# Kernel optimization log

Hardware: AMD Instinct MI355X
Metric: run time of the kernel (lower is better)

## Reference

```python
import jax, jax.numpy as jnp
import numpy as np

B, T, I, H = 64, 1024, 256, 256

def setup_inputs() -> dict:
    key = jax.random.key(0)
    ks = jax.random.split(key, 7)
    inputs = jax.random.normal(ks[0], (B * T, I), jnp.float32)
    states = jax.random.normal(ks[1], (B, 1, H), jnp.float32)  # [B, num_layers, H]
    mask = (jax.random.uniform(ks[2], (B, T, 1, 1)) < 0.9).astype(jnp.float32)
    s = 1.0 / np.sqrt(H)  # PyTorch RNN init scale
    W_ih = jax.random.uniform(ks[3], (3 * H, I), jnp.float32, -s, s)
    W_hh = jax.random.uniform(ks[4], (3 * H, H), jnp.float32, -s, s)
    b_ih = jax.random.uniform(ks[5], (3 * H,), jnp.float32, -s, s)
    b_hh = jax.random.uniform(ks[6], (3 * H,), jnp.float32, -s, s)
    return dict(inputs=inputs, states=states, mask=mask,
                W_ih=W_ih, W_hh=W_hh, b_ih=b_ih, b_hh=b_hh, seq_len=T)

def reference(inputs, states, mask, W_ih, W_hh, b_ih, b_hh, seq_len):
    # inputs: [B*T, I] -> [B, T, I]
    x = inputs.reshape(-1, seq_len, inputs.shape[-1])
    m = mask[..., 0, 0]                      # [B, T]
    # pre-loop blend: hs = states * mask[:, 0]
    h0 = states[:, 0, :] * m[:, 0:1]         # [B, H]
    xs = jnp.swapaxes(x, 0, 1)               # [T, B, I]
    ms = jnp.swapaxes(m, 0, 1)[..., None]    # [T, B, 1]

    def step(h, xm):
        x_t, m_t = xm
        gi = x_t @ W_ih.T + b_ih             # [B, 3H]
        gh = h @ W_hh.T + b_hh               # [B, 3H]
        ir, iz, i_n = jnp.split(gi, 3, axis=-1)
        hr, hz, h_n = jnp.split(gh, 3, axis=-1)
        r = jax.nn.sigmoid(ir + hr)
        z = jax.nn.sigmoid(iz + hz)
        n = jnp.tanh(i_n + r * h_n)
        nh = (1.0 - z) * n + z * h           # GRU new hidden = step output
        h_new = h * (1.0 - m_t) + nh * m_t   # masked state blend
        return h_new, nh

    h_fin, ys = jax.lax.scan(step, h0, (xs, ms))
    x_out = jnp.swapaxes(ys, 0, 1).reshape(-1, ys.shape[-1])  # [B*T, H]
    state_out = h_fin[:, None, :]                              # [B, 1, H]
    return (x_out, state_out)
```

## Files before the change

### kernel.cpp

```cpp
#include <hip/hip_runtime.h>

typedef unsigned int u32;
typedef __fp16 f16;
typedef __fp16 h2 __attribute__((ext_vector_type(2)));
typedef __fp16 h8 __attribute__((ext_vector_type(8)));
typedef float f32x2v __attribute__((ext_vector_type(2)));
typedef float f32x4v __attribute__((ext_vector_type(4)));
typedef float f32x16v __attribute__((ext_vector_type(16)));
typedef u32 u32x4v __attribute__((ext_vector_type(4)));

static constexpr int BB = 64;
static constexpr int TT = 1024;
static constexpr int HH = 256;
static constexpr int GG = 768;
static constexpr size_t GI_BYTES = (size_t)BB * TT * GG * 2;

__device__ __forceinline__ u32 pk2(float a, float b) {
  h2 r = __builtin_amdgcn_cvt_pkrtz(a, b);
  return __builtin_bit_cast(u32, r);
}
__device__ __forceinline__ float fdot2u(u32 a, u32 b, float c) {
  return __builtin_amdgcn_fdot2(__builtin_bit_cast(h2, a), __builtin_bit_cast(h2, b), c, false);
}
__device__ __forceinline__ float dpp_x1(float x) {
  return __builtin_bit_cast(float,
      __builtin_amdgcn_mov_dpp(__builtin_bit_cast(int, x), 0xB1, 0xF, 0xF, true));
}
__device__ __forceinline__ float sigf(float x) { return 1.f / (1.f + __expf(-x)); }
__device__ __forceinline__ float tanhf2(float x) {
  float e = __expf(2.f * x);
  return 1.f - 2.f / (e + 1.f);
}

__global__ void prepack_whh(const float* __restrict__ Whh, u32* __restrict__ Wp) {
  int id = blockIdx.x * 256 + threadIdx.x;
  int v = id >> 9;
  int j = id & 511;
  int u = j >> 1, kh = j & 1;
  int g = v >> 6, d = v & 63;
  int row = g * 256 + u;
  int k0 = 128 * kh + 2 * d;
  const float* p = Whh + (size_t)row * HH + k0;
  Wp[id] = pk2(p[0], p[1]);
}

__device__ __forceinline__ f32x16v zero16() {
  f32x16v z;
#pragma unroll
  for (int i = 0; i < 16; ++i) z[i] = 0.f;
  return z;
}

__global__ __launch_bounds__(256, 2) void gemm_gi(
    const float* __restrict__ x, const float* __restrict__ Wih,
    const float* __restrict__ bih, f16* __restrict__ gi) {
  __shared__ u32 bl[16384];
  const int tid = threadIdx.x;
  const int lane = tid & 63;
  const int wv = tid >> 6;
  const int wr = wv >> 1, wc = wv & 1;
  const int l31 = lane & 31, lh = lane >> 5;
  const int m0 = blockIdx.x << 7;

  u32x4v afr[2][16];
#pragma unroll
  for (int fr = 0; fr < 2; ++fr) {
#pragma unroll
    for (int km = 0; km < 16; ++km) {
      int row = m0 + wr * 64 + fr * 32 + l31;
      int k0 = km * 16 + lh * 8;
      const f32x4v* p = (const f32x4v*)(x + (size_t)row * 256 + k0);
      f32x4v u = p[0], v = p[1];
      u32x4v t;
      t.x = pk2(u.x, u.y); t.y = pk2(u.z, u.w);
      t.z = pk2(v.x, v.y); t.w = pk2(v.z, v.w);
      afr[fr][km] = t;
    }
  }

  for (int nt = 0; nt < 6; ++nt) {
    const int n0 = nt << 7;
#pragma unroll
    for (int i = 0; i < 64; ++i) {
      int idx = i * 256 + tid;
      int r = idx >> 7, wd = idx & 127;
      const f32x2v* g = (const f32x2v*)(Wih + (size_t)(n0 + r) * 256 + 2 * wd);
      f32x2v f = *g;
      bl[r * 128 + (wd ^ ((r & 15) << 2))] = pk2(f.x, f.y);
    }
    __syncthreads();

    f32x16v acc00 = zero16(), acc01 = zero16(), acc10 = zero16(), acc11 = zero16();
#pragma unroll
    for (int km = 0; km < 16; ++km) {
      int w0 = km * 8 + lh * 4;
      int rc0 = wc * 64 + l31;
      int rc1 = wc * 64 + 32 + l31;
      u32x4v b0 = *(const u32x4v*)&bl[rc0 * 128 + (w0 ^ ((rc0 & 15) << 2))];
      u32x4v b1 = *(const u32x4v*)&bl[rc1 * 128 + (w0 ^ ((rc1 & 15) << 2))];
      h8 a0h = __builtin_bit_cast(h8, afr[0][km]);
      h8 a1h = __builtin_bit_cast(h8, afr[1][km]);
      h8 b0h = __builtin_bit_cast(h8, b0);
      h8 b1h = __builtin_bit_cast(h8, b1);
      acc00 = __builtin_amdgcn_mfma_f32_32x32x16_f16(a0h, b0h, acc00, 0, 0, 0);
      acc10 = __builtin_amdgcn_mfma_f32_32x32x16_f16(a1h, b0h, acc10, 0, 0, 0);
      acc01 = __builtin_amdgcn_mfma_f32_32x32x16_f16(a0h, b1h, acc01, 0, 0, 0);
      acc11 = __builtin_amdgcn_mfma_f32_32x32x16_f16(a1h, b1h, acc11, 0, 0, 0);
    }

#define EPI(ACC, FR, FC)                                                      \
    {                                                                         \
      int gc = n0 + wc * 64 + (FC) * 32 + l31;                                \
      float bias = bih[gc];                                                   \
      _Pragma("unroll")                                                       \
      for (int rg = 0; rg < 16; ++rg) {                                       \
        int gr = m0 + wr * 64 + (FR) * 32 + 4 * lh + (rg & 3) + 8 * (rg >> 2);\
        gi[(size_t)gr * 768 + gc] = (f16)(ACC[rg] + bias);                    \
      }                                                                       \
    }
    EPI(acc00, 0, 0) EPI(acc10, 1, 0) EPI(acc01, 0, 1) EPI(acc11, 1, 1)
#undef EPI
    __syncthreads();
  }
}

__global__ __launch_bounds__(512, 2) void recur(
    const u32* __restrict__ Wp, const f16* __restrict__ gi,
    const float* __restrict__ states, const float* __restrict__ mask,
    const float* __restrict__ bhh_g, float* __restrict__ out) {
  const int b = blockIdx.x;
  const int j = threadIdx.x;
  const int u = j >> 1;
  const int kh = j & 1;

  __shared__ u32 hbuf[2][128];
  __shared__ float mlds[TT];

  u32 w[192];
#pragma unroll
  for (int v = 0; v < 192; ++v) w[v] = Wp[(size_t)v * 512 + j];
#pragma unroll
  for (int v = 0; v < 192; ++v) asm volatile("" : "+v"(w[v]));

  const float bhr = bhh_g[u];
  const float bhz = bhh_g[256 + u];
  const float bhn = bhh_g[512 + u];

  const float* mk = mask + b * TT;
  const f16* gib = gi + (size_t)b * TT * GG;
  float* outb = out + (size_t)b * TT * HH;

  for (int i = j; i < TT; i += 512) mlds[i] = mk[i];

  float hreg = states[b * HH + u] * mk[0];
  if (kh == 0) ((f16*)hbuf[0])[u] = (f16)hreg;
  __syncthreads();

  f16 gr_c = gib[u], gz_c = gib[256 + u], gn_c = gib[512 + u];
  float nh_prev = 0.f;

  for (int t = 0; t < TT; ++t) {
    int tn = (t + 1 < TT) ? (t + 1) : (TT - 1);
    const f16* gnp = gib + (size_t)tn * GG;
    f16 gr_n = gnp[u], gz_n = gnp[256 + u], gn_n = gnp[512 + u];
    if (t > 0 && kh == 0) outb[(size_t)(t - 1) * HH + u] = nh_prev;

    const float mt = mlds[t];
    const u32x4v* hq = (const u32x4v*)&hbuf[t & 1][kh << 6];

    float ar0 = 0.f, ar1 = 0.f, az0 = 0.f, az1 = 0.f, an0 = 0.f, an1 = 0.f;
#pragma unroll
    for (int gp = 0; gp < 16; ++gp) {
      u32x4v q = hq[gp];
      const int v = gp * 4;
      ar0 = fdot2u(w[v + 0], q.x, ar0);
      az0 = fdot2u(w[64 + v + 0], q.x, az0);
      an0 = fdot2u(w[128 + v + 0], q.x, an0);
      ar1 = fdot2u(w[v + 1], q.y, ar1);
      az1 = fdot2u(w[64 + v + 1], q.y, az1);
      an1 = fdot2u(w[128 + v + 1], q.y, an1);
      ar0 = fdot2u(w[v + 2], q.z, ar0);
      az0 = fdot2u(w[64 + v + 2], q.z, az0);
      an0 = fdot2u(w[128 + v + 2], q.z, an0);
      ar1 = fdot2u(w[v + 3], q.w, ar1);
      az1 = fdot2u(w[64 + v + 3], q.w, az1);
      an1 = fdot2u(w[128 + v + 3], q.w, an1);
    }
    float ghr = ar0 + ar1, ghz = az0 + az1, ghn = an0 + an1;
    ghr += dpp_x1(ghr); ghz += dpp_x1(ghz); ghn += dpp_x1(ghn);
    ghr += bhr; ghz += bhz; ghn += bhn;

    float r = sigf((float)gr_c + ghr);
    float z = sigf((float)gz_c + ghz);
    float n = tanhf2((float)gn_c + r * ghn);
    float nh = (1.f - z) * n + z * hreg;
    float hnew = hreg * (1.f - mt) + nh * mt;
    nh_prev = nh;
    hreg = hnew;
    if (kh == 0) ((f16*)hbuf[(t + 1) & 1])[u] = (f16)hnew;
    gr_c = gr_n; gz_c = gz_n; gn_c = gn_n;
    __syncthreads();
  }

  if (kh == 0) {
    outb[(size_t)(TT - 1) * HH + u] = nh_prev;
    out[(size_t)BB * TT * HH + b * HH + u] = hreg;
  }
}

extern "C" void kernel_launch(void* const* d_in, const int* in_sizes, int n_in,
                              void* d_out, int out_size, void* d_ws, size_t ws_size,
                              hipStream_t stream) {
  const float* x      = (const float*)d_in[0];
  const float* states = (const float*)d_in[1];
  const float* mask   = (const float*)d_in[2];
  const float* W_ih   = (const float*)d_in[3];
  const float* W_hh   = (const float*)d_in[4];
  const float* b_ih   = (const float*)d_in[5];
  const float* b_hh   = (const float*)d_in[6];
  float* out = (float*)d_out;

  char* ws = (char*)d_ws;
  f16* gi = (f16*)ws;
  u32* Wp = (u32*)(ws + GI_BYTES);

  prepack_whh<<<dim3(384), dim3(256), 0, stream>>>(W_hh, Wp);
  gemm_gi<<<dim3(512), dim3(256), 0, stream>>>(x, W_ih, b_ih, gi);
  recur<<<dim3(64), dim3(512), 0, stream>>>(Wp, gi, states, mask, b_hh, out);
}
```

Baseline: 1.541 ms.

## Batch eight sequences per block and compute recurrent GEMV with MFMA

The recurrent kernel now handles 8 batch rows per block (8 blocks instead of 64). The h·W_hh product becomes 16x16x32 f16 MFMA instructions with W_hh prepacked into AGPR-resident fragments, replacing per-thread fdot2 chains. The r/z recurrent biases are folded into the input GEMM epilogue, and the W_ih staging load is widened to float4. The intent is to cut per-step dot-product cost by using matrix units. The trade-off is only 8 active CUs and more per-step work per block, all still serialized on the recurrence.

```diff
diff --git a/kernel.cpp b/kernel.cpp
--- a/kernel.cpp
+++ b/kernel.cpp
@@ -3,10 +3,12 @@
 typedef unsigned int u32;
 typedef __fp16 f16;
 typedef __fp16 h2 __attribute__((ext_vector_type(2)));
+typedef __fp16 h4 __attribute__((ext_vector_type(4)));
 typedef __fp16 h8 __attribute__((ext_vector_type(8)));
 typedef float f32x2v __attribute__((ext_vector_type(2)));
 typedef float f32x4v __attribute__((ext_vector_type(4)));
 typedef float f32x16v __attribute__((ext_vector_type(16)));
+typedef u32 u32x2v __attribute__((ext_vector_type(2)));
 typedef u32 u32x4v __attribute__((ext_vector_type(4)));
 
 static constexpr int BB = 64;
@@ -19,12 +21,9 @@
   h2 r = __builtin_amdgcn_cvt_pkrtz(a, b);
   return __builtin_bit_cast(u32, r);
 }
-__device__ __forceinline__ float fdot2u(u32 a, u32 b, float c) {
-  return __builtin_amdgcn_fdot2(__builtin_bit_cast(h2, a), __builtin_bit_cast(h2, b), c, false);
-}
-__device__ __forceinline__ float dpp_x1(float x) {
+__device__ __forceinline__ float dpp_shr8(float x) {
   return __builtin_bit_cast(float,
-      __builtin_amdgcn_mov_dpp(__builtin_bit_cast(int, x), 0xB1, 0xF, 0xF, true));
+      __builtin_amdgcn_mov_dpp(__builtin_bit_cast(int, x), 0x118, 0xF, 0xF, true));
 }
 __device__ __forceinline__ float sigf(float x) { return 1.f / (1.f + __expf(-x)); }
 __device__ __forceinline__ float tanhf2(float x) {
@@ -32,16 +31,19 @@
   return 1.f - 2.f / (e + 1.f);
 }
 
-__global__ void prepack_whh(const float* __restrict__ Whh, u32* __restrict__ Wp) {
+__global__ void prepack_wa(const float* __restrict__ Whh, u32* __restrict__ Wa) {
   int id = blockIdx.x * 256 + threadIdx.x;
-  int v = id >> 9;
-  int j = id & 511;
-  int u = j >> 1, kh = j & 1;
-  int g = v >> 6, d = v & 63;
-  int row = g * 256 + u;
-  int k0 = 128 * kh + 2 * d;
-  const float* p = Whh + (size_t)row * HH + k0;
-  Wp[id] = pk2(p[0], p[1]);
+  int lane_g = id / 192;
+  int rrem = id - lane_g * 192;
+  int i = rrem >> 2, e2 = rrem & 3;
+  int ti6 = i >> 3, ks = i & 7;
+  int G = ti6 >> 1, tj = ti6 & 1;
+  int w = lane_g >> 6, l = lane_g & 63;
+  int m = G * 16 + 2 * w + tj;
+  int row = 16 * m + (l & 15);
+  int k = 32 * ks + 8 * (l >> 4) + 2 * e2;
+  const float* p = Whh + (size_t)row * HH + k;
+  Wa[id] = pk2(p[0], p[1]);
 }
 
 __device__ __forceinline__ f32x16v zero16() {
@@ -53,7 +55,8 @@
 
 __global__ __launch_bounds__(256, 2) void gemm_gi(
     const float* __restrict__ x, const float* __restrict__ Wih,
-    const float* __restrict__ bih, f16* __restrict__ gi) {
+    const float* __restrict__ bih, const float* __restrict__ bhh,
+    f16* __restrict__ gi) {
   __shared__ u32 bl[16384];
   const int tid = threadIdx.x;
   const int lane = tid & 63;
@@ -81,12 +84,16 @@
   for (int nt = 0; nt < 6; ++nt) {
     const int n0 = nt << 7;
 #pragma unroll
-    for (int i = 0; i < 64; ++i) {
-      int idx = i * 256 + tid;
-      int r = idx >> 7, wd = idx & 127;
-      const f32x2v* g = (const f32x2v*)(Wih + (size_t)(n0 + r) * 256 + 2 * wd);
-      f32x2v f = *g;
-      bl[r * 128 + (wd ^ ((r & 15) << 2))] = pk2(f.x, f.y);
+    for (int it = 0; it < 32; ++it) {
+      int flat = it * 256 + tid;
+      int r = flat >> 6;
+      int q = flat & 63;
+      f32x4v f = *(const f32x4v*)(Wih + (size_t)(n0 + r) * 256 + 4 * q);
+      u32x2v pw;
+      pw.x = pk2(f.x, f.y);
+      pw.y = pk2(f.z, f.w);
+      int wd = 2 * q;
+      *(u32x2v*)&bl[r * 128 + (wd ^ ((r & 15) << 2))] = pw;
     }
     __syncthreads();
 
@@ -111,7 +118,7 @@
 #define EPI(ACC, FR, FC)                                                      \
     {                                                                         \
       int gc = n0 + wc * 64 + (FC) * 32 + l31;                                \
-      float bias = bih[gc];                                                   \
+      float bias = bih[gc] + (gc < 512 ? bhh[gc] : 0.f);                      \
       _Pragma("unroll")                                                       \
       for (int rg = 0; rg < 16; ++rg) {                                       \
         int gr = m0 + wr * 64 + (FR) * 32 + 4 * lh + (rg & 3) + 8 * (rg >> 2);\
@@ -125,87 +132,117 @@
 }
 
 __global__ __launch_bounds__(512, 2) void recur(
-    const u32* __restrict__ Wp, const f16* __restrict__ gi,
+    const u32* __restrict__ Wa, const f16* __restrict__ gi,
     const float* __restrict__ states, const float* __restrict__ mask,
     const float* __restrict__ bhh_g, float* __restrict__ out) {
-  const int b = blockIdx.x;
-  const int j = threadIdx.x;
-  const int u = j >> 1;
-  const int kh = j & 1;
-
-  __shared__ u32 hbuf[2][128];
-  __shared__ float mlds[TT];
-
-  u32 w[192];
-#pragma unroll
-  for (int v = 0; v < 192; ++v) w[v] = Wp[(size_t)v * 512 + j];
-#pragma unroll
-  for (int v = 0; v < 192; ++v) asm volatile("" : "+v"(w[v]));
-
-  const float bhr = bhh_g[u];
-  const float bhz = bhh_g[256 + u];
-  const float bhn = bhh_g[512 + u];
-
-  const float* mk = mask + b * TT;
-  const f16* gib = gi + (size_t)b * TT * GG;
-  float* outb = out + (size_t)b * TT * HH;
-
-  for (int i = j; i < TT; i += 512) mlds[i] = mk[i];
-
-  float hreg = states[b * HH + u] * mk[0];
-  if (kh == 0) ((f16*)hbuf[0])[u] = (f16)hreg;
+  const int blk = blockIdx.x;
+  const int tid = threadIdx.x;
+  const int w = tid >> 6, l = tid & 63;
+  const int lr = l & 15, g = l >> 4;
+  const int c = lr & 7, tj = lr >> 3;
+  const int u0 = 32 * w + 16 * tj + 4 * g;
+
+  __shared__ __align__(16) f16 hb[2][4096];
+  __shared__ f16 mlds[8192];
+
+  u32x4v wa[48];
+  {
+    const u32x4v* wap = (const u32x4v*)Wa + (size_t)(w * 64 + l) * 48;
+#pragma unroll
+    for (int i = 0; i < 48; ++i) wa[i] = wap[i];
+#pragma unroll
+    for (int i = 0; i < 48; ++i) asm volatile("" : "+a"(wa[i]));
+  }
+
+  for (int idx = tid; idx < 8192; idx += 512) {
+    int b8 = idx >> 10, tt = idx & 1023;
+    mlds[tt * 8 + b8] = (f16)mask[(size_t)(blk * 8 + b8) * TT + tt];
+  }
+  for (int idx = tid; idx < 4096; idx += 512) {
+    int unit = idx >> 4, cc = idx & 15;
+    float v = 0.f;
+    if (cc < 8)
+      v = states[(size_t)(blk * 8 + cc) * HH + unit] *
+          mask[(size_t)(blk * 8 + cc) * TT];
+    int fa = (unit >> 5) * 512 + ((unit >> 3) & 3) * 128 + cc * 8 + (unit & 7);
+    hb[0][fa] = (f16)v;
+    hb[1][fa] = (f16)v;
+  }
+
+  const f16* gip = gi + (size_t)(blk * 8 + c) * TT * GG + u0;
+  float* outp = out + (size_t)(blk * 8 + c) * TT * HH + u0;
+
+  float hreg[4];
+  {
+    float m0 = mask[(size_t)(blk * 8 + c) * TT];
+    const f32x4v s4 = *(const f32x4v*)(states + (size_t)(blk * 8 + c) * HH + u0);
+#pragma unroll
+    for (int r = 0; r < 4; ++r) hreg[r] = s4[r] * m0;
+  }
+  const f32x4v bn4 = *(const f32x4v*)(bhh_g + 512 + u0);
+
+  const int wbase = w * 512 + ((2 * tj + (g >> 1)) & 3) * 128 + c * 8 + 4 * (g & 1);
+  const int rbase = g * 128 + lr * 8;
+
+  f32x4v nhp = {0.f, 0.f, 0.f, 0.f};
   __syncthreads();
 
-  f16 gr_c = gib[u], gz_c = gib[256 + u], gn_c = gib[512 + u];
-  float nh_prev = 0.f;
-
   for (int t = 0; t < TT; ++t) {
-    int tn = (t + 1 < TT) ? (t + 1) : (TT - 1);
-    const f16* gnp = gib + (size_t)tn * GG;
-    f16 gr_n = gnp[u], gz_n = gnp[256 + u], gn_n = gnp[512 + u];
-    if (t > 0 && kh == 0) outb[(size_t)(t - 1) * HH + u] = nh_prev;
-
-    const float mt = mlds[t];
-    const u32x4v* hq = (const u32x4v*)&hbuf[t & 1][kh << 6];
-
-    float ar0 = 0.f, ar1 = 0.f, az0 = 0.f, az1 = 0.f, an0 = 0.f, an1 = 0.f;
-#pragma unroll
-    for (int gp = 0; gp < 16; ++gp) {
-      u32x4v q = hq[gp];
-      const int v = gp * 4;
-      ar0 = fdot2u(w[v + 0], q.x, ar0);
-      az0 = fdot2u(w[64 + v + 0], q.x, az0);
-      an0 = fdot2u(w[128 + v + 0], q.x, an0);
-      ar1 = fdot2u(w[v + 1], q.y, ar1);
-      az1 = fdot2u(w[64 + v + 1], q.y, az1);
-      an1 = fdot2u(w[128 + v + 1], q.y, an1);
-      ar0 = fdot2u(w[v + 2], q.z, ar0);
-      az0 = fdot2u(w[64 + v + 2], q.z, az0);
-      an0 = fdot2u(w[128 + v + 2], q.z, an0);
-      ar1 = fdot2u(w[v + 3], q.w, ar1);
-      az1 = fdot2u(w[64 + v + 3], q.w, az1);
-      an1 = fdot2u(w[128 + v + 3], q.w, an1);
-    }
-    float ghr = ar0 + ar1, ghz = az0 + az1, ghn = an0 + an1;
-    ghr += dpp_x1(ghr); ghz += dpp_x1(ghz); ghn += dpp_x1(ghn);
-    ghr += bhr; ghz += bhz; ghn += bhn;
-
-    float r = sigf((float)gr_c + ghr);
-    float z = sigf((float)gz_c + ghz);
-    float n = tanhf2((float)gn_c + r * ghn);
-    float nh = (1.f - z) * n + z * hreg;
-    float hnew = hreg * (1.f - mt) + nh * mt;
-    nh_prev = nh;
-    hreg = hnew;
-    if (kh == 0) ((f16*)hbuf[(t + 1) & 1])[u] = (f16)hnew;
-    gr_c = gr_n; gz_c = gz_n; gn_c = gn_n;
+    if (t > 0) *(f32x4v*)(outp + (size_t)(t - 1) * HH) = nhp;
+    const h4 ldA = *(const h4*)(gip + (size_t)t * GG);
+    const h4 ldB = *(const h4*)(gip + (size_t)t * GG + 256);
+    const h4 ldC = *(const h4*)(gip + (size_t)t * GG + 512);
+    const float mt = (float)mlds[t * 8 + c];
+
+    const u32x4v* bp = (const u32x4v*)&hb[t & 1][rbase];
+    f32x4v a0 = {0.f, 0.f, 0.f, 0.f}, a1 = a0, a2 = a0, a3 = a0, a4 = a0, a5 = a0;
+    u32x4v bf = bp[0];
+#pragma unroll
+    for (int ks = 0; ks < 8; ++ks) {
+      u32x4v bnx = bp[((ks + 1) & 7) * 64];
+      h8 bh = __builtin_bit_cast(h8, bf);
+      a0 = __builtin_amdgcn_mfma_f32_16x16x32_f16(__builtin_bit_cast(h8, wa[ks]),      bh, a0, 0, 0, 0);
+      a1 = __builtin_amdgcn_mfma_f32_16x16x32_f16(__builtin_bit_cast(h8, wa[8 + ks]),  bh, a1, 0, 0, 0);
+      a2 = __builtin_amdgcn_mfma_f32_16x16x32_f16(__builtin_bit_cast(h8, wa[16 + ks]), bh, a2, 0, 0, 0);
+      a3 = __builtin_amdgcn_mfma_f32_16x16x32_f16(__builtin_bit_cast(h8, wa[24 + ks]), bh, a3, 0, 0, 0);
+      a4 = __builtin_amdgcn_mfma_f32_16x16x32_f16(__builtin_bit_cast(h8, wa[32 + ks]), bh, a4, 0, 0, 0);
+      a5 = __builtin_amdgcn_mfma_f32_16x16x32_f16(__builtin_bit_cast(h8, wa[40 + ks]), bh, a5, 0, 0, 0);
+      bf = bnx;
+    }
+
+    const bool hi = (lr >= 8);
+    f32x4v vr, vz, vn;
+#pragma unroll
+    for (int r = 0; r < 4; ++r) {
+      float d0 = dpp_shr8(a1[r]);
+      float d1 = dpp_shr8(a3[r]);
+      float d2 = dpp_shr8(a5[r]);
+      vr[r] = hi ? d0 : a0[r];
+      vz[r] = hi ? d1 : a2[r];
+      vn[r] = hi ? d2 : a4[r];
+    }
+
+#pragma unroll
+    for (int r = 0; r < 4; ++r) {
+      float rr = sigf((float)ldA[r] + vr[r]);
+      float zz = sigf((float)ldB[r] + vz[r]);
+      float nn = tanhf2((float)ldC[r] + rr * (vn[r] + bn4[r]));
+      float nh = zz * (hreg[r] - nn) + nn;
+      hreg[r] = hreg[r] + mt * (nh - hreg[r]);
+      nhp[r] = nh;
+    }
+    u32x2v hp;
+    hp.x = pk2(hreg[0], hreg[1]);
+    hp.y = pk2(hreg[2], hreg[3]);
+    *(u32x2v*)&hb[(t + 1) & 1][wbase] = hp;
     __syncthreads();
   }
 
-  if (kh == 0) {
-    outb[(size_t)(TT - 1) * HH + u] = nh_prev;
-    out[(size_t)BB * TT * HH + b * HH + u] = hreg;
-  }
+  *(f32x4v*)(outp + (size_t)(TT - 1) * HH) = nhp;
+  f32x4v hf;
+#pragma unroll
+  for (int r = 0; r < 4; ++r) hf[r] = hreg[r];
+  *(f32x4v*)(out + (size_t)BB * TT * HH + (size_t)(blk * 8 + c) * HH + u0) = hf;
 }
 
 extern "C" void kernel_launch(void* const* d_in, const int* in_sizes, int n_in,
@@ -222,9 +259,9 @@
 
   char* ws = (char*)d_ws;
   f16* gi = (f16*)ws;
-  u32* Wp = (u32*)(ws + GI_BYTES);
-
-  prepack_whh<<<dim3(384), dim3(256), 0, stream>>>(W_hh, Wp);
-  gemm_gi<<<dim3(512), dim3(256), 0, stream>>>(x, W_ih, b_ih, gi);
-  recur<<<dim3(64), dim3(512), 0, stream>>>(Wp, gi, states, mask, b_hh, out);
-}
+  u32* Wa = (u32*)(ws + GI_BYTES);
+
+  prepack_wa<<<dim3(384), dim3(256), 0, stream>>>(W_hh, Wa);
+  gemm_gi<<<dim3(512), dim3(256), 0, stream>>>(x, W_ih, b_ih, b_hh, gi);
+  recur<<<dim3(8), dim3(512), 0, stream>>>(Wa, gi, states, mask, b_hh, out);
+}
```

After: 2.739 ms. 1.78x slower.

## Pin recurrent weights to fixed VGPRs via inline asm and fold biases into GEMM

Applied to the files above, without the earlier changes.

The recurrent kernel now loads its 192 packed W_hh words per thread straight into hard-wired VGPRs v64-v255 with inline-asm dwordx4 loads. The dot products are written as inline v_dot2 asm, so the compiler can no longer spill or shuffle the weights, and the per-thread weight layout is repacked to be contiguous for wide loads. The r/z hidden biases are folded into the input GEMM epilogue, the GRU blend math is simplified, and the W_ih staging loads are widened to float4. The software prefetch of next-step gi values is removed, so each step now loads gi on the critical path. Relying on fixed register numbers with clobbers is fragile and may conflict with compiler allocation.

```diff
diff --git a/kernel.cpp b/kernel.cpp
--- a/kernel.cpp
+++ b/kernel.cpp
@@ -1,12 +1,14 @@
 #include <hip/hip_runtime.h>
 
 typedef unsigned int u32;
+typedef unsigned long long u64;
 typedef __fp16 f16;
 typedef __fp16 h2 __attribute__((ext_vector_type(2)));
 typedef __fp16 h8 __attribute__((ext_vector_type(8)));
 typedef float f32x2v __attribute__((ext_vector_type(2)));
 typedef float f32x4v __attribute__((ext_vector_type(4)));
 typedef float f32x16v __attribute__((ext_vector_type(16)));
+typedef u32 u32x2v __attribute__((ext_vector_type(2)));
 typedef u32 u32x4v __attribute__((ext_vector_type(4)));
 
 static constexpr int BB = 64;
@@ -19,9 +21,6 @@
   h2 r = __builtin_amdgcn_cvt_pkrtz(a, b);
   return __builtin_bit_cast(u32, r);
 }
-__device__ __forceinline__ float fdot2u(u32 a, u32 b, float c) {
-  return __builtin_amdgcn_fdot2(__builtin_bit_cast(h2, a), __builtin_bit_cast(h2, b), c, false);
-}
 __device__ __forceinline__ float dpp_x1(float x) {
   return __builtin_bit_cast(float,
       __builtin_amdgcn_mov_dpp(__builtin_bit_cast(int, x), 0xB1, 0xF, 0xF, true));
@@ -32,16 +31,14 @@
   return 1.f - 2.f / (e + 1.f);
 }
 
-__global__ void prepack_whh(const float* __restrict__ Whh, u32* __restrict__ Wp) {
+__global__ void prepack_whh(const float* __restrict__ Whh, u32* __restrict__ Wp2) {
   int id = blockIdx.x * 256 + threadIdx.x;
-  int v = id >> 9;
-  int j = id & 511;
+  int j = id / 192;
+  int rem = id - j * 192;
+  int G = rem >> 6, d = rem & 63;
   int u = j >> 1, kh = j & 1;
-  int g = v >> 6, d = v & 63;
-  int row = g * 256 + u;
-  int k0 = 128 * kh + 2 * d;
-  const float* p = Whh + (size_t)row * HH + k0;
-  Wp[id] = pk2(p[0], p[1]);
+  const float* p = Whh + (size_t)(G * 256 + u) * HH + 128 * kh + 2 * d;
+  Wp2[id] = pk2(p[0], p[1]);
 }
 
 __device__ __forceinline__ f32x16v zero16() {
@@ -53,7 +50,8 @@
 
 __global__ __launch_bounds__(256, 2) void gemm_gi(
     const float* __restrict__ x, const float* __restrict__ Wih,
-    const float* __restrict__ bih, f16* __restrict__ gi) {
+    const float* __restrict__ bih, const float* __restrict__ bhh,
+    f16* __restrict__ gi) {
   __shared__ u32 bl[16384];
   const int tid = threadIdx.x;
   const int lane = tid & 63;
@@ -81,12 +79,16 @@
   for (int nt = 0; nt < 6; ++nt) {
     const int n0 = nt << 7;
 #pragma unroll
-    for (int i = 0; i < 64; ++i) {
-      int idx = i * 256 + tid;
-      int r = idx >> 7, wd = idx & 127;
-      const f32x2v* g = (const f32x2v*)(Wih + (size_t)(n0 + r) * 256 + 2 * wd);
-      f32x2v f = *g;
-      bl[r * 128 + (wd ^ ((r & 15) << 2))] = pk2(f.x, f.y);
+    for (int it = 0; it < 32; ++it) {
+      int flat = it * 256 + tid;
+      int r = flat >> 6;
+      int q = flat & 63;
+      f32x4v f = *(const f32x4v*)(Wih + (size_t)(n0 + r) * 256 + 4 * q);
+      u32x2v pw;
+      pw.x = pk2(f.x, f.y);
+      pw.y = pk2(f.z, f.w);
+      int wd = 2 * q;
+      *(u32x2v*)&bl[r * 128 + (wd ^ ((r & 15) << 2))] = pw;
     }
     __syncthreads();
 
@@ -111,7 +113,7 @@
 #define EPI(ACC, FR, FC)                                                      \
     {                                                                         \
       int gc = n0 + wc * 64 + (FC) * 32 + l31;                                \
-      float bias = bih[gc];                                                   \
+      float bias = bih[gc] + (gc < 512 ? bhh[gc] : 0.f);                      \
       _Pragma("unroll")                                                       \
       for (int rg = 0; rg < 16; ++rg) {                                       \
         int gr = m0 + wr * 64 + (FR) * 32 + 4 * lh + (rg & 3) + 8 * (rg >> 2);\
@@ -124,8 +126,54 @@
   }
 }
 
+#define WCLOB \
+  "v64","v65","v66","v67","v68","v69","v70","v71", \
+  "v72","v73","v74","v75","v76","v77","v78","v79", \
+  "v80","v81","v82","v83","v84","v85","v86","v87", \
+  "v88","v89","v90","v91","v92","v93","v94","v95", \
+  "v96","v97","v98","v99","v100","v101","v102","v103", \
+  "v104","v105","v106","v107","v108","v109","v110","v111", \
+  "v112","v113","v114","v115","v116","v117","v118","v119", \
+  "v120","v121","v122","v123","v124","v125","v126","v127", \
+  "v128","v129","v130","v131","v132","v133","v134","v135", \
+  "v136","v137","v138","v139","v140","v141","v142","v143", \
+  "v144","v145","v146","v147","v148","v149","v150","v151", \
+  "v152","v153","v154","v155","v156","v157","v158","v159", \
+  "v160","v161","v162","v163","v164","v165","v166","v167", \
+  "v168","v169","v170","v171","v172","v173","v174","v175", \
+  "v176","v177","v178","v179","v180","v181","v182","v183", \
+  "v184","v185","v186","v187","v188","v189","v190","v191", \
+  "v192","v193","v194","v195","v196","v197","v198","v199", \
+  "v200","v201","v202","v203","v204","v205","v206","v207", \
+  "v208","v209","v210","v211","v212","v213","v214","v215", \
+  "v216","v217","v218","v219","v220","v221","v222","v223", \
+  "v224","v225","v226","v227","v228","v229","v230","v231", \
+  "v232","v233","v234","v235","v236","v237","v238","v239", \
+  "v240","v241","v242","v243","v244","v245","v246","v247", \
+  "v248","v249","v250","v251","v252","v253","v254","v255"
+
+#define LD16(A,B,OFF) "global_load_dwordx4 v[" #A ":" #B "], %0, off offset:" #OFF "\n\t"
+
+#define DOTG(R0,R1,R2,R3,Z0,Z1,Z2,Z3,N0,N1,N2,N3,Q)          \
+  asm volatile(                                              \
+    "v_dot2_f32_f16 %0, v" #R0 ", %3, %0\n\t"                \
+    "v_dot2_f32_f16 %1, v" #Z0 ", %3, %1\n\t"                \
+    "v_dot2_f32_f16 %2, v" #N0 ", %3, %2\n\t"                \
+    "v_dot2_f32_f16 %0, v" #R1 ", %4, %0\n\t"                \
+    "v_dot2_f32_f16 %1, v" #Z1 ", %4, %1\n\t"                \
+    "v_dot2_f32_f16 %2, v" #N1 ", %4, %2\n\t"                \
+    "v_dot2_f32_f16 %0, v" #R2 ", %5, %0\n\t"                \
+    "v_dot2_f32_f16 %1, v" #Z2 ", %5, %1\n\t"                \
+    "v_dot2_f32_f16 %2, v" #N2 ", %5, %2\n\t"                \
+    "v_dot2_f32_f16 %0, v" #R3 ", %6, %0\n\t"                \
+    "v_dot2_f32_f16 %1, v" #Z3 ", %6, %1\n\t"                \
+    "v_dot2_f32_f16 %2, v" #N3 ", %6, %2\n\t"                \
+    : "+v"(ar), "+v"(az), "+v"(an)                           \
+    : "v"((Q).x), "v"((Q).y), "v"((Q).z), "v"((Q).w)         \
+    : WCLOB)
+
 __global__ __launch_bounds__(512, 2) void recur(
-    const u32* __restrict__ Wp, const f16* __restrict__ gi,
+    const u32* __restrict__ Wp2, const f16* __restrict__ gi,
     const float* __restrict__ states, const float* __restrict__ mask,
     const float* __restrict__ bhh_g, float* __restrict__ out) {
   const int b = blockIdx.x;
@@ -133,72 +181,80 @@
   const int u = j >> 1;
   const int kh = j & 1;
 
-  __shared__ u32 hbuf[2][128];
+  __shared__ __align__(16) u32 hbuf[2][128];
   __shared__ float mlds[TT];
 
-  u32 w[192];
-#pragma unroll
-  for (int v = 0; v < 192; ++v) w[v] = Wp[(size_t)v * 512 + j];
-#pragma unroll
-  for (int v = 0; v < 192; ++v) asm volatile("" : "+v"(w[v]));
-
-  const float bhr = bhh_g[u];
-  const float bhz = bhh_g[256 + u];
   const float bhn = bhh_g[512 + u];
 
   const float* mk = mask + b * TT;
-  const f16* gib = gi + (size_t)b * TT * GG;
+  const f16* gcur = gi + (size_t)b * TT * GG + u;
   float* outb = out + (size_t)b * TT * HH;
 
   for (int i = j; i < TT; i += 512) mlds[i] = mk[i];
 
   float hreg = states[b * HH + u] * mk[0];
   if (kh == 0) ((f16*)hbuf[0])[u] = (f16)hreg;
+
+  {
+    u64 wa = (u64)(Wp2 + (size_t)j * 192);
+    asm volatile(
+      LD16(64,67,0)    LD16(68,71,16)   LD16(72,75,32)   LD16(76,79,48)
+      LD16(80,83,64)   LD16(84,87,80)   LD16(88,91,96)   LD16(92,95,112)
+      LD16(96,99,128)  LD16(100,103,144) LD16(104,107,160) LD16(108,111,176)
+      LD16(112,115,192) LD16(116,119,208) LD16(120,123,224) LD16(124,127,240)
+      LD16(128,131,256) LD16(132,135,272) LD16(136,139,288) LD16(140,143,304)
+      LD16(144,147,320) LD16(148,151,336) LD16(152,155,352) LD16(156,159,368)
+      LD16(160,163,384) LD16(164,167,400) LD16(168,171,416) LD16(172,175,432)
+      LD16(176,179,448) LD16(180,183,464) LD16(184,187,480) LD16(188,191,496)
+      LD16(192,195,512) LD16(196,199,528) LD16(200,203,544) LD16(204,207,560)
+      LD16(208,211,576) LD16(212,215,592) LD16(216,219,608) LD16(220,223,624)
+      LD16(224,227,640) LD16(228,231,656) LD16(232,235,672) LD16(236,239,688)
+      LD16(240,243,704) LD16(244,247,720) LD16(248,251,736) LD16(252,255,752)
+      "s_waitcnt vmcnt(0)\n\t"
+      :: "v"(wa) : WCLOB, "memory");
+  }
   __syncthreads();
 
-  f16 gr_c = gib[u], gz_c = gib[256 + u], gn_c = gib[512 + u];
   float nh_prev = 0.f;
 
   for (int t = 0; t < TT; ++t) {
-    int tn = (t + 1 < TT) ? (t + 1) : (TT - 1);
-    const f16* gnp = gib + (size_t)tn * GG;
-    f16 gr_n = gnp[u], gz_n = gnp[256 + u], gn_n = gnp[512 + u];
     if (t > 0 && kh == 0) outb[(size_t)(t - 1) * HH + u] = nh_prev;
-
+    f16 gr_c = gcur[0], gz_c = gcur[256], gn_c = gcur[512];
     const float mt = mlds[t];
+
     const u32x4v* hq = (const u32x4v*)&hbuf[t & 1][kh << 6];
-
-    float ar0 = 0.f, ar1 = 0.f, az0 = 0.f, az1 = 0.f, an0 = 0.f, an1 = 0.f;
-#pragma unroll
-    for (int gp = 0; gp < 16; ++gp) {
-      u32x4v q = hq[gp];
-      const int v = gp * 4;
-      ar0 = fdot2u(w[v + 0], q.x, ar0);
-      az0 = fdot2u(w[64 + v + 0], q.x, az0);
-      an0 = fdot2u(w[128 + v + 0], q.x, an0);
-      ar1 = fdot2u(w[v + 1], q.y, ar1);
-      az1 = fdot2u(w[64 + v + 1], q.y, az1);
-      an1 = fdot2u(w[128 + v + 1], q.y, an1);
-      ar0 = fdot2u(w[v + 2], q.z, ar0);
-      az0 = fdot2u(w[64 + v + 2], q.z, az0);
-      an0 = fdot2u(w[128 + v + 2], q.z, an0);
-      ar1 = fdot2u(w[v + 3], q.w, ar1);
-      az1 = fdot2u(w[64 + v + 3], q.w, az1);
-      an1 = fdot2u(w[128 + v + 3], q.w, an1);
-    }
-    float ghr = ar0 + ar1, ghz = az0 + az1, ghn = an0 + an1;
-    ghr += dpp_x1(ghr); ghz += dpp_x1(ghz); ghn += dpp_x1(ghn);
-    ghr += bhr; ghz += bhz; ghn += bhn;
+    float ar = 0.f, az = 0.f, an = 0.f;
+
+    { u32x4v q = hq[0];  DOTG(64,65,66,67,    128,129,130,131, 192,193,194,195, q); }
+    { u32x4v q = hq[1];  DOTG(68,69,70,71,    132,133,134,135, 196,197,198,199, q); }
+    { u32x4v q = hq[2];  DOTG(72,73,74,75,    136,137,138,139, 200,201,202,203, q); }
+    { u32x4v q = hq[3];  DOTG(76,77,78,79,    140,141,142,143, 204,205,206,207, q); }
+    { u32x4v q = hq[4];  DOTG(80,81,82,83,    144,145,146,147, 208,209,210,211, q); }
+    { u32x4v q = hq[5];  DOTG(84,85,86,87,    148,149,150,151, 212,213,214,215, q); }
+    { u32x4v q = hq[6];  DOTG(88,89,90,91,    152,153,154,155, 216,217,218,219, q); }
+    { u32x4v q = hq[7];  DOTG(92,93,94,95,    156,157,158,159, 220,221,222,223, q); }
+    { u32x4v q = hq[8];  DOTG(96,97,98,99,    160,161,162,163, 224,225,226,227, q); }
+    { u32x4v q = hq[9];  DOTG(100,101,102,103, 164,165,166,167, 228,229,230,231, q); }
+    { u32x4v q = hq[10]; DOTG(104,105,106,107, 168,169,170,171, 232,233,234,235, q); }
+    { u32x4v q = hq[11]; DOTG(108,109,110,111, 172,173,174,175, 236,237,238,239, q); }
+    { u32x4v q = hq[12]; DOTG(112,113,114,115, 176,177,178,179, 240,241,242,243, q); }
+    { u32x4v q = hq[13]; DOTG(116,117,118,119, 180,181,182,183, 244,245,246,247, q); }
+    { u32x4v q = hq[14]; DOTG(120,121,122,123, 184,185,186,187, 248,249,250,251, q); }
+    { u32x4v q = hq[15]; DOTG(124,125,126,127, 188,189,190,191, 252,253,254,255, q); }
+
+    float ghr = ar + dpp_x1(ar);
+    float ghz = az + dpp_x1(az);
+    float ghn = an + dpp_x1(an);
 
     float r = sigf((float)gr_c + ghr);
     float z = sigf((float)gz_c + ghz);
-    float n = tanhf2((float)gn_c + r * ghn);
-    float nh = (1.f - z) * n + z * hreg;
-    float hnew = hreg * (1.f - mt) + nh * mt;
+    float n = tanhf2((float)gn_c + r * (ghn + bhn));
+    float nh = z * (hreg - n) + n;
+    float hnew = hreg + mt * (nh - hreg);
     nh_prev = nh;
     hreg = hnew;
     if (kh == 0) ((f16*)hbuf[(t + 1) & 1])[u] = (f16)hnew;
-    gr_c = gr_n; gz_c = gz_n; gn_c = gn_n;
+    gcur += GG;
     __syncthreads();
   }
 
@@ -222,9 +278,9 @@
 
   char* ws = (char*)d_ws;
   f16* gi = (f16*)ws;
-  u32* Wp = (u32*)(ws + GI_BYTES);
-
-  prepack_whh<<<dim3(384), dim3(256), 0, stream>>>(W_hh, Wp);
-  gemm_gi<<<dim3(512), dim3(256), 0, stream>>>(x, W_ih, b_ih, gi);
-  recur<<<dim3(64), dim3(512), 0, stream>>>(Wp, gi, states, mask, b_hh, out);
-}
+  u32* Wp2 = (u32*)(ws + GI_BYTES);
+
+  prepack_whh<<<dim3(384), dim3(256), 0, stream>>>(W_hh, Wp2);
+  gemm_gi<<<dim3(512), dim3(256), 0, stream>>>(x, W_ih, b_ih, b_hh, gi);
+  recur<<<dim3(64), dim3(512), 0, stream>>>(Wp2, gi, states, mask, b_hh, out);
+}
```

New measurement: 1.379 ms. 1.12x faster.
